# Performance work log

Measured on AMD Instinct MI355X. Metric: run time of the kernel, lower is better.

Reference implementation:

```python
import jax, jax.numpy as jnp
import numpy as np

B, S, H, NH = 2, 2048, 1024, 16
HD = H // NH
ROTARY_DIM = 64
EPS = 1e-5
MINUS_INF = -10000.0


def _apply_rotary(q, k, rotary_dim):
    # q, k: [B, S, NH, HD]; GPT-NeoX style rotate_half on first rotary_dim dims
    pos = jnp.arange(S, dtype=jnp.float32)
    inv_freq = 1.0 / (10000.0 ** (jnp.arange(0, rotary_dim, 2, dtype=jnp.float32) / rotary_dim))
    freqs = pos[:, None] * inv_freq[None, :]                      # [S, rd/2]
    cos = jnp.concatenate([jnp.cos(freqs)] * 2, -1)[None, :, None, :]  # [1,S,1,rd]
    sin = jnp.concatenate([jnp.sin(freqs)] * 2, -1)[None, :, None, :]

    def rot(t):
        t_rot, t_pass = t[..., :rotary_dim], t[..., rotary_dim:]
        t1, t2 = jnp.split(t_rot, 2, axis=-1)
        rotated = jnp.concatenate([-t2, t1], axis=-1)
        return jnp.concatenate([t_rot * cos + rotated * sin, t_pass], axis=-1)

    return rot(q), rot(k)


def setup_inputs() -> dict:
    key = jax.random.key(0)
    ks = jax.random.split(key, 6)
    w_scale = 0.02
    return {
        "x": jax.random.normal(ks[0], (B, S, H), jnp.float32),
        "input_mask": jnp.ones((B, S), jnp.int32),
        "norm_w": jnp.ones((H,), jnp.float32),
        "norm_b": jnp.zeros((H,), jnp.float32),
        "attn_qkvw": jax.random.normal(ks[1], (H, 3 * H), jnp.float32) * w_scale,
        "attn_qkvb": jax.random.normal(ks[2], (3 * H,), jnp.float32) * w_scale,
        "attn_ow": jax.random.normal(ks[3], (H, H), jnp.float32) * w_scale,
        "attn_ob": jax.random.normal(ks[4], (H,), jnp.float32) * w_scale,
    }


def reference(x, input_mask, norm_w, norm_b, attn_qkvw, attn_qkvb, attn_ow, attn_ob):
    # pre-layernorm (qkv_gemm path with config.pre_layer_norm)
    mu = x.mean(-1, keepdims=True)
    var = x.var(-1, keepdims=True)
    xn = (x - mu) * jax.lax.rsqrt(var + EPS) * norm_w + norm_b

    # fused QKV projection
    qkv = xn @ attn_qkvw + attn_qkvb                       # [B,S,3H]
    q, k, v = jnp.split(qkv, 3, axis=-1)
    q = q.reshape(B, S, NH, HD)
    k = k.reshape(B, S, NH, HD)
    v = v.reshape(B, S, NH, HD)

    # rotary embedding on q,k
    q, k = _apply_rotary(q, k, ROTARY_DIM)

    # scaled scores + mask bias (1 - mask) * -10000 + triangular masking
    scale = 1.0 / np.sqrt(HD).astype(np.float32)
    scores = jnp.einsum("bqhd,bkhd->bhqk", q, k) * scale   # [B,NH,S,S]
    mask_bias = (1.0 - input_mask.astype(scores.dtype)) * MINUS_INF
    scores = scores + mask_bias[:, None, None, :]
    causal = jnp.tril(jnp.ones((S, S), bool))
    scores = jnp.where(causal[None, None], scores, MINUS_INF)

    probs = jax.nn.softmax(scores, axis=-1)
    ctx = jnp.einsum("bhqk,bkhd->bqhd", probs, v).reshape(B, S, H)

    # output projection (vector_matmul + bias)
    return ctx @ attn_ow + attn_ob
```

## Files before the change

kernel.cpp:

```cpp
#include <hip/hip_runtime.h>
#include <hip/hip_bf16.h>

#define B_  2
#define S_  2048
#define H_  1024
#define NH_ 16
#define HD_ 64
#define T_  (B_*S_)
#define H3_ (3*H_)

typedef float  floatx4 __attribute__((ext_vector_type(4)));
typedef __bf16 bf16x8  __attribute__((ext_vector_type(8)));

__device__ inline unsigned short f2bf_rn(float f) {
    union { float f; unsigned int u; } v; v.f = f;
    unsigned int u = v.u;
    u += 0x7fffu + ((u >> 16) & 1u);
    return (unsigned short)(u >> 16);
}
__device__ inline floatx4 fzero4() { floatx4 v; v[0]=0.f; v[1]=0.f; v[2]=0.f; v[3]=0.f; return v; }

__device__ inline float bf2f(unsigned short u) {
    union { unsigned int i; float f; } x; x.i = ((unsigned int)u) << 16; return x.f;
}

__device__ inline unsigned int cvtpk_bf16(float lo, float hi) {
    unsigned int r;
    asm("v_cvt_pk_bf16_f32 %0, %1, %2" : "=v"(r) : "v"(lo), "v"(hi));
    return r;
}

__device__ inline void gload_lds16(const unsigned short* g, unsigned short* l) {
    __builtin_amdgcn_global_load_lds((const __attribute__((address_space(1))) unsigned int*)g,
                                     (__attribute__((address_space(3))) unsigned int*)l,
                                     16, 0, 0);
}

#define TLD 72
__global__ __launch_bounds__(256) void pre_k(const float* __restrict__ qkvw,
                                             const float* __restrict__ ow,
                                             unsigned short* __restrict__ qkvwT,
                                             unsigned short* __restrict__ owT,
                                             const float* __restrict__ x,
                                             const float* __restrict__ nw,
                                             const float* __restrict__ nb,
                                             unsigned short* __restrict__ xn) {
    const int tid = threadIdx.x;
    if (blockIdx.x < 1024) {
        __shared__ unsigned short Ts[64 * TLD];
        int id = blockIdx.x;
        const float* W; unsigned short* Wt; int N, nbs, kb;
        if (id < 768) { W = qkvw; Wt = qkvwT; N = H3_; nbs = (id % 48) * 64; kb = (id / 48) * 64; }
        else { id -= 768; W = ow; Wt = owT; N = H_; nbs = (id % 16) * 64; kb = (id / 16) * 64; }
        const int K = H_;
        #pragma unroll
        for (int p = 0; p < 4; p++) {
            const int krow = kb + p * 16 + (tid >> 4);
            const int ncol = (tid & 15) * 4;
            const float4 w = *reinterpret_cast<const float4*>(&W[(size_t)krow * N + nbs + ncol]);
            Ts[(ncol + 0) * TLD + p * 16 + (tid >> 4)] = f2bf_rn(w.x);
            Ts[(ncol + 1) * TLD + p * 16 + (tid >> 4)] = f2bf_rn(w.y);
            Ts[(ncol + 2) * TLD + p * 16 + (tid >> 4)] = f2bf_rn(w.z);
            Ts[(ncol + 3) * TLD + p * 16 + (tid >> 4)] = f2bf_rn(w.w);
        }
        __syncthreads();
        #pragma unroll
        for (int p = 0; p < 2; p++) {
            const int n = (tid >> 3) + p * 32;
            const int k8 = (tid & 7) * 8;
            const uint4 v = *reinterpret_cast<const uint4*>(&Ts[n * TLD + k8]);
            *reinterpret_cast<uint4*>(&Wt[(size_t)(nbs + n) * K + kb + k8]) = v;
        }
    } else {
        const int t = blockIdx.x - 1024;
        const float4 v = reinterpret_cast<const float4*>(x + (size_t)t * H_)[tid];
        float s  = v.x + v.y + v.z + v.w;
        float s2 = v.x*v.x + v.y*v.y + v.z*v.z + v.w*v.w;
        for (int off = 32; off > 0; off >>= 1) {
            s  += __shfl_down(s,  off, 64);
            s2 += __shfl_down(s2, off, 64);
        }
        __shared__ float red[8];
        const int wave = tid >> 6, lane = tid & 63;
        if (lane == 0) { red[wave] = s; red[4 + wave] = s2; }
        __syncthreads();
        if (tid == 0) {
            red[0] = red[0] + red[1] + red[2] + red[3];
            red[4] = red[4] + red[5] + red[6] + red[7];
        }
        __syncthreads();
        const float mean = red[0] * (1.f / H_);
        const float var  = red[4] * (1.f / H_) - mean * mean;
        const float rstd = rsqrtf(var + 1e-5f);
        const float4 wv = reinterpret_cast<const float4*>(nw)[tid];
        const float4 bv = reinterpret_cast<const float4*>(nb)[tid];
        ushort4 o = make_ushort4(f2bf_rn((v.x - mean) * rstd * wv.x + bv.x),
                                 f2bf_rn((v.y - mean) * rstd * wv.y + bv.y),
                                 f2bf_rn((v.z - mean) * rstd * wv.z + bv.z),
                                 f2bf_rn((v.w - mean) * rstd * wv.w + bv.w));
        reinterpret_cast<ushort4*>(xn + (size_t)t * H_)[tid] = o;
    }
}

__global__ __launch_bounds__(256) void gemm_qkv_k(const unsigned short* __restrict__ A,
                                                  const unsigned short* __restrict__ Bt,
                                                  const float* __restrict__ bias,
                                                  unsigned short* __restrict__ Qo,
                                                  unsigned short* __restrict__ Ko,
                                                  unsigned short* __restrict__ Vto) {
    __shared__ unsigned short As0[128 * 32], As1[128 * 32];
    __shared__ unsigned short Bs0[ 64 * 32], Bs1[ 64 * 32];

    const int tid  = threadIdx.x;
    const int lane = tid & 63;
    const int wave = tid >> 6;
    const int mBase = blockIdx.y * 128;
    const int nBase = blockIdx.x * 64;
    const int K = H_;

    const int srow = lane >> 2;
    const int scol = (lane & 3) * 8;
    const int mrow = lane & 15;
    const int koff = (lane >> 4) * 8;

    floatx4 acc[2][4];
    #pragma unroll
    for (int i = 0; i < 2; i++)
        #pragma unroll
        for (int j = 0; j < 4; j++) acc[i][j] = fzero4();

    for (int kb = 0; kb < K; kb += 64) {
        __syncthreads();
        #pragma unroll
        for (int p = 0; p < 2; p++) {
            const int r = wave * 16 + p * 64;
            const size_t ga = (size_t)(mBase + r + srow) * K + kb + scol;
            gload_lds16(&A[ga],      &As0[r * 32]);
            gload_lds16(&A[ga + 32], &As1[r * 32]);
        }
        {
            const int r = wave * 16;
            const size_t gb = (size_t)(nBase + r + srow) * K + kb + scol;
            gload_lds16(&Bt[gb],      &Bs0[r * 32]);
            gload_lds16(&Bt[gb + 32], &Bs1[r * 32]);
        }
        __syncthreads();

        #pragma unroll
        for (int half = 0; half < 2; half++) {
            const unsigned short* As = half ? As1 : As0;
            const unsigned short* Bs = half ? Bs1 : Bs0;
            bf16x8 afrag[2], bfrag[4];
            #pragma unroll
            for (int mt = 0; mt < 2; mt++)
                afrag[mt] = *reinterpret_cast<const bf16x8*>(&As[(wave * 32 + mt * 16 + mrow) * 32 + koff]);
            #pragma unroll
            for (int nt = 0; nt < 4; nt++)
                bfrag[nt] = *reinterpret_cast<const bf16x8*>(&Bs[(nt * 16 + mrow) * 32 + koff]);
            #pragma unroll
            for (int mt = 0; mt < 2; mt++)
                #pragma unroll
                for (int nt = 0; nt < 4; nt++)
                    acc[mt][nt] = __builtin_amdgcn_mfma_f32_16x16x32_bf16(afrag[mt], bfrag[nt], acc[mt][nt], 0, 0, 0);
        }
    }

    const int col0 = lane & 15;
    const int r0   = (lane >> 4) * 4;
    const int hg   = nBase >> 6;
    const int sec  = hg >> 4;
    const int h    = hg & 15;

    float bs[4];
    #pragma unroll
    for (int nt = 0; nt < 4; nt++) bs[nt] = bias[nBase + nt * 16 + col0];

    if (sec < 2) {
        unsigned short* dst = (sec == 0) ? Qo : Ko;
        const float if0 = __expf((float)col0        * (-0.2878231366f));
        const float if1 = __expf((float)(16 + col0) * (-0.2878231366f));
        #pragma unroll
        for (int mt = 0; mt < 2; mt++) {
            #pragma unroll
            for (int reg = 0; reg < 4; reg++) {
                const int t  = mBase + wave * 32 + mt * 16 + r0 + reg;
                const int bb = t >> 11;
                const int s  = t & (S_ - 1);
                float sn0, cs0, sn1, cs1;
                __sincosf((float)s * if0, &sn0, &cs0);
                __sincosf((float)s * if1, &sn1, &cs1);
                const float v0 = acc[mt][0][reg] + bs[0];
                const float v1 = acc[mt][1][reg] + bs[1];
                const float v2 = acc[mt][2][reg] + bs[2];
                const float v3 = acc[mt][3][reg] + bs[3];
                const float o0 = v0 * cs0 - v2 * sn0;
                const float o1 = v1 * cs1 - v3 * sn1;
                const float o2 = v2 * cs0 + v0 * sn0;
                const float o3 = v3 * cs1 + v1 * sn1;
                const size_t rb = ((size_t)(bb * NH_ + h) * S_ + s) * HD_;
                dst[rb +      col0] = f2bf_rn(o0);
                dst[rb + 16 + col0] = f2bf_rn(o1);
                dst[rb + 32 + col0] = f2bf_rn(o2);
                dst[rb + 48 + col0] = f2bf_rn(o3);
            }
        }
    } else {
        #pragma unroll
        for (int mt = 0; mt < 2; mt++) {
            const int t0 = mBase + wave * 32 + mt * 16 + r0;
            const int bb = t0 >> 11;
            const int s0 = t0 & (S_ - 1);
            #pragma unroll
            for (int nt = 0; nt < 4; nt++) {
                const int d = nt * 16 + col0;
                ushort4 o;
                o.x = f2bf_rn(acc[mt][nt][0] + bs[nt]);
                o.y = f2bf_rn(acc[mt][nt][1] + bs[nt]);
                o.z = f2bf_rn(acc[mt][nt][2] + bs[nt]);
                o.w = f2bf_rn(acc[mt][nt][3] + bs[nt]);
                *reinterpret_cast<ushort4*>(&Vto[((size_t)(bb * NH_ + h) * HD_ + d) * S_ + s0]) = o;
            }
        }
    }
}

__global__ __launch_bounds__(256) void gemm_proj_k(const unsigned short* __restrict__ A,
                                                   const unsigned short* __restrict__ Bt,
                                                   const float* __restrict__ bias,
                                                   float* __restrict__ Cf,
                                                   int M, int N, int K) {
    __shared__ unsigned short As0[128 * 32], As1[128 * 32];
    __shared__ unsigned short Bs0[ 64 * 32], Bs1[ 64 * 32];

    const int tid  = threadIdx.x;
    const int lane = tid & 63;
    const int wave = tid >> 6;
    const int id  = blockIdx.x;
    const int nid = (id & 7) * 64 + (id >> 3);
    const int mBase = (nid >> 4) * 128;
    const int nBase = (nid & 15) * 64;

    const int srow = lane >> 2;
    const int scol = (lane & 3) * 8;
    const int mrow = lane & 15;
    const int koff = (lane >> 4) * 8;

    floatx4 acc[2][4];
    #pragma unroll
    for (int i = 0; i < 2; i++)
        #pragma unroll
        for (int j = 0; j < 4; j++) acc[i][j] = fzero4();

    for (int kb = 0; kb < K; kb += 64) {
        __syncthreads();
        #pragma unroll
        for (int p = 0; p < 2; p++) {
            const int r = wave * 16 + p * 64;
            const size_t ga = (size_t)(mBase + r + srow) * K + kb + scol;
            gload_lds16(&A[ga],      &As0[r * 32]);
            gload_lds16(&A[ga + 32], &As1[r * 32]);
        }
        {
            const int r = wave * 16;
            const size_t gb = (size_t)(nBase + r + srow) * K + kb + scol;
            gload_lds16(&Bt[gb],      &Bs0[r * 32]);
            gload_lds16(&Bt[gb + 32], &Bs1[r * 32]);
        }
        __syncthreads();

        #pragma unroll
        for (int half = 0; half < 2; half++) {
            const unsigned short* As = half ? As1 : As0;
            const unsigned short* Bs = half ? Bs1 : Bs0;
            bf16x8 afrag[2], bfrag[4];
            #pragma unroll
            for (int mt = 0; mt < 2; mt++)
                afrag[mt] = *reinterpret_cast<const bf16x8*>(&As[(wave * 32 + mt * 16 + mrow) * 32 + koff]);
            #pragma unroll
            for (int nt = 0; nt < 4; nt++)
                bfrag[nt] = *reinterpret_cast<const bf16x8*>(&Bs[(nt * 16 + mrow) * 32 + koff]);
            #pragma unroll
            for (int mt = 0; mt < 2; mt++)
                #pragma unroll
                for (int nt = 0; nt < 4; nt++)
                    acc[mt][nt] = __builtin_amdgcn_mfma_f32_16x16x32_bf16(afrag[mt], bfrag[nt], acc[mt][nt], 0, 0, 0);
        }
    }

    const int col0 = lane & 15;
    const int r0   = (lane >> 4) * 4;
    #pragma unroll
    for (int mt = 0; mt < 2; mt++) {
        #pragma unroll
        for (int nt = 0; nt < 4; nt++) {
            const int gcol = nBase + nt * 16 + col0;
            const float bsv = bias[gcol];
            #pragma unroll
            for (int reg = 0; reg < 4; reg++) {
                const int grow = mBase + wave * 32 + mt * 16 + r0 + reg;
                Cf[(size_t)grow * N + gcol] = acc[mt][nt][reg] + bsv;
            }
        }
    }
}

#define ALD 72
#define SCL2 0.1803368801f
#define MNEG -14427.0f

__global__ __launch_bounds__(256, 4) void attn_k(const unsigned short* __restrict__ Q,
                                                 const unsigned short* __restrict__ Kg,
                                                 const unsigned short* __restrict__ Vt,
                                                 const int* __restrict__ mask,
                                                 unsigned short* __restrict__ ctx) {
    const int id = blockIdx.x;
    const int bh = id & 31;
    const int v  = 31 - (id >> 5);
    const int b  = bh >> 4;
    const int h  = bh & 15;
    const int tid  = threadIdx.x;
    const int lane = tid & 63;
    const int wave = tid >> 6;

    __shared__ unsigned short Ks [2][64 * ALD];
    __shared__ unsigned short Vts[2][64 * ALD];
    __shared__ unsigned short Mb [S_];

    const size_t base = (size_t)bh * S_ * HD_;
    const int qbase = v * 64 + wave * 16;
    const int r16  = lane & 15;
    const int koff = (lane >> 4) * 8;
    const int g8   = (lane >> 4) * 8;
    const int qcol = qbase + r16;

    {
        const int k0 = tid * 8;
        const int4 ma = *reinterpret_cast<const int4*>(&mask[b * S_ + k0]);
        const int4 mc = *reinterpret_cast<const int4*>(&mask[b * S_ + k0 + 4]);
        union { unsigned short us[8]; uint4 q; } pk;
        pk.us[0] = f2bf_rn((1.f - (float)ma.x) * MNEG);
        pk.us[1] = f2bf_rn((1.f - (float)ma.y) * MNEG);
        pk.us[2] = f2bf_rn((1.f - (float)ma.z) * MNEG);
        pk.us[3] = f2bf_rn((1.f - (float)ma.w) * MNEG);
        pk.us[4] = f2bf_rn((1.f - (float)mc.x) * MNEG);
        pk.us[5] = f2bf_rn((1.f - (float)mc.y) * MNEG);
        pk.us[6] = f2bf_rn((1.f - (float)mc.z) * MNEG);
        pk.us[7] = f2bf_rn((1.f - (float)mc.w) * MNEG);
        *reinterpret_cast<uint4*>(&Mb[k0]) = pk.q;
    }

    const bf16x8 qf0 = *reinterpret_cast<const bf16x8*>(&Q[base + (size_t)(qbase + r16) * HD_ + koff]);
    const bf16x8 qf1 = *reinterpret_cast<const bf16x8*>(&Q[base + (size_t)(qbase + r16) * HD_ + 32 + koff]);

    bf16x8 onesA;
    #pragma unroll
    for (int q = 0; q < 8; q++) onesA[q] = (__bf16)1.f;

    floatx4 Ot[4];
    #pragma unroll
    for (int db = 0; db < 4; db++) Ot[db] = fzero4();
    floatx4 Lacc = fzero4();

    const int srow = tid >> 3;
    const int scol = (tid & 7) * 8;
    const int pi = ((srow & 12) << 1) | (srow & 3) | (((srow >> 4) & 1) << 2);

    uint4 k00, k01, k10, k11, v00, v01, v10, v11;
#define PF_TILE(TT, KR0, KR1, VR0, VR1) do {                                                   \
        const int kb_ = (TT) * 64;                                                             \
        KR0 = *reinterpret_cast<const uint4*>(&Kg[base + (size_t)(kb_ + pi)      * HD_ + scol]); \
        KR1 = *reinterpret_cast<const uint4*>(&Kg[base + (size_t)(kb_ + 32 + pi) * HD_ + scol]); \
        VR0 = *reinterpret_cast<const uint4*>(&Vt[base + (size_t)srow        * S_ + kb_ + scol]);  \
        VR1 = *reinterpret_cast<const uint4*>(&Vt[base + (size_t)(srow + 32) * S_ + kb_ + scol]);  \
    } while (0)
#define PREFETCH_MACRO(MI) do {                                                                \
        const int t0_ = min(2 * (MI), v);                                                      \
        const int t1_ = min(2 * (MI) + 1, v);                                                  \
        PF_TILE(t0_, k00, k01, v00, v01);                                                      \
        PF_TILE(t1_, k10, k11, v10, v11);                                                      \
    } while (0)

    const int nmac = (v + 2) >> 1;
    PREFETCH_MACRO(0);

    for (int mi = 0; mi < nmac; mi++) {
        if (mi) __syncthreads();
        *reinterpret_cast<uint4*>(&Ks [0][ srow       * ALD + scol]) = k00;
        *reinterpret_cast<uint4*>(&Ks [0][(srow + 32) * ALD + scol]) = k01;
        *reinterpret_cast<uint4*>(&Ks [1][ srow       * ALD + scol]) = k10;
        *reinterpret_cast<uint4*>(&Ks [1][(srow + 32) * ALD + scol]) = k11;
        *reinterpret_cast<uint4*>(&Vts[0][ srow       * ALD + scol]) = v00;
        *reinterpret_cast<uint4*>(&Vts[0][(srow + 32) * ALD + scol]) = v01;
        *reinterpret_cast<uint4*>(&Vts[1][ srow       * ALD + scol]) = v10;
        *reinterpret_cast<uint4*>(&Vts[1][(srow + 32) * ALD + scol]) = v11;
        __syncthreads();
        if (mi + 1 < nmac) PREFETCH_MACRO(mi + 1);

        #pragma unroll
        for (int half = 0; half < 2; half++) {
            const int kt = 2 * mi + half;
            if (half && kt > v) continue;
            const int kb = kt * 64;
            const unsigned short* ks = Ks [half];
            const unsigned short* vs = Vts[half];

            const unsigned short* mbp = &Mb[kb + g8];
            const ushort4 b00 = *reinterpret_cast<const ushort4*>(mbp);
            const ushort4 b01 = *reinterpret_cast<const ushort4*>(mbp + 4);
            const ushort4 b10 = *reinterpret_cast<const ushort4*>(mbp + 32);
            const ushort4 b11 = *reinterpret_cast<const ushort4*>(mbp + 36);

            #pragma unroll
            for (int w = 0; w < 2; w++) {
                float p[2][4];
                #pragma unroll
                for (int ab = 0; ab < 2; ab++) {
                    const int nt = w * 2 + ab;
                    const bf16x8 kf0 = *reinterpret_cast<const bf16x8*>(&ks[(nt * 16 + r16) * ALD + koff]);
                    const bf16x8 kf1 = *reinterpret_cast<const bf16x8*>(&ks[(nt * 16 + r16) * ALD + 32 + koff]);
                    floatx4 c = fzero4();
                    c = __builtin_amdgcn_mfma_f32_16x16x32_bf16(kf0, qf0, c, 0, 0, 0);
                    c = __builtin_amdgcn_mfma_f32_16x16x32_bf16(kf1, qf1, c, 0, 0, 0);
                    const ushort4 bb = w ? (ab ? b11 : b10) : (ab ? b01 : b00);
                    const int kbase = kb + w * 32 + ab * 4 + g8;
                    float sc0 = c[0] * SCL2 + bf2f(bb.x);
                    float sc1 = c[1] * SCL2 + bf2f(bb.y);
                    float sc2 = c[2] * SCL2 + bf2f(bb.z);
                    float sc3 = c[3] * SCL2 + bf2f(bb.w);
                    if (kt == v) {
                        if (kbase + 0 > qcol) sc0 = MNEG;
                        if (kbase + 1 > qcol) sc1 = MNEG;
                        if (kbase + 2 > qcol) sc2 = MNEG;
                        if (kbase + 3 > qcol) sc3 = MNEG;
                    }
                    p[ab][0] = exp2f(sc0);
                    p[ab][1] = exp2f(sc1);
                    p[ab][2] = exp2f(sc2);
                    p[ab][3] = exp2f(sc3);
                }
                union { uint4 u; bf16x8 v; } pf;
                pf.u.x = cvtpk_bf16(p[0][0], p[0][1]);
                pf.u.y = cvtpk_bf16(p[0][2], p[0][3]);
                pf.u.z = cvtpk_bf16(p[1][0], p[1][1]);
                pf.u.w = cvtpk_bf16(p[1][2], p[1][3]);
                __builtin_amdgcn_s_setprio(1);
                #pragma unroll
                for (int db = 0; db < 4; db++) {
                    const bf16x8 vf = *reinterpret_cast<const bf16x8*>(&vs[(db * 16 + r16) * ALD + w * 32 + koff]);
                    Ot[db] = __builtin_amdgcn_mfma_f32_16x16x32_bf16(vf, pf.v, Ot[db], 0, 0, 0);
                }
                Lacc = __builtin_amdgcn_mfma_f32_16x16x32_bf16(onesA, pf.v, Lacc, 0, 0, 0);
                __builtin_amdgcn_s_setprio(0);
            }
        }
    }
#undef PREFETCH_MACRO
#undef PF_TILE

    const float rl = 1.f / Lacc[0];
    const int r4 = (lane >> 4) * 4;
    #pragma unroll
    for (int db = 0; db < 4; db++) {
        ushort4 o;
        o.x = f2bf_rn(Ot[db][0] * rl);
        o.y = f2bf_rn(Ot[db][1] * rl);
        o.z = f2bf_rn(Ot[db][2] * rl);
        o.w = f2bf_rn(Ot[db][3] * rl);
        *reinterpret_cast<ushort4*>(&ctx[((size_t)b * S_ + qcol) * H_ + h * HD_ + db * 16 + r4]) = o;
    }
}

extern "C" void kernel_launch(void* const* d_in, const int* in_sizes, int n_in,
                              void* d_out, int out_size, void* d_ws, size_t ws_size,
                              hipStream_t stream) {
    const float* x     = (const float*)d_in[0];
    const int*   mask  = (const int*)d_in[1];
    const float* normw = (const float*)d_in[2];
    const float* normb = (const float*)d_in[3];
    const float* qkvw  = (const float*)d_in[4];
    const float* qkvb  = (const float*)d_in[5];
    const float* ow    = (const float*)d_in[6];
    const float* ob    = (const float*)d_in[7];
    float* out = (float*)d_out;

    char* ws = (char*)d_ws;
    unsigned short* xn_bf   = (unsigned short*)(ws);
    unsigned short* qkvwT   = (unsigned short*)(ws + (8ull  << 20));
    unsigned short* owT     = (unsigned short*)(ws + (14ull << 20));
    unsigned short* Qb      = (unsigned short*)(ws + (16ull << 20));
    unsigned short* Kb      = (unsigned short*)(ws + (24ull << 20));
    unsigned short* Vtb     = (unsigned short*)(ws + (32ull << 20));
    unsigned short* ctx_bf  = (unsigned short*)(ws + (40ull << 20));

    pre_k<<<1024 + T_, 256, 0, stream>>>(qkvw, ow, qkvwT, owT, x, normw, normb, xn_bf);
    gemm_qkv_k<<<dim3(H3_ / 64, T_ / 128), 256, 0, stream>>>(xn_bf, qkvwT, qkvb, Qb, Kb, Vtb);
    attn_k<<<1024, 256, 0, stream>>>(Qb, Kb, Vtb, mask, ctx_bf);
    gemm_proj_k<<<512, 256, 0, stream>>>(ctx_bf, owT, ob, out, T_, H_, H_);
}
```

Baseline: 185.7 us.

## Fuse all stages into one persistent cooperative kernel with grid syncs

```diff
diff --git a/kernel.cpp b/kernel.cpp
--- a/kernel.cpp
+++ b/kernel.cpp
@@ -1,5 +1,8 @@
 #include <hip/hip_runtime.h>
 #include <hip/hip_bf16.h>
+#include <hip/hip_cooperative_groups.h>
+
+namespace cg = cooperative_groups;
 
 #define B_  2
 #define S_  2048
@@ -37,6 +40,458 @@
 }
 
 #define TLD 72
+#define ALD 72
+#define SCL2 0.1803368801f
+#define MNEG -14427.0f
+
+__device__ unsigned int g_tk[3];
+
+__global__ __launch_bounds__(256, 4) void fused_k(
+        const float* __restrict__ qkvw, const float* __restrict__ ow,
+        unsigned short* __restrict__ qkvwT, unsigned short* __restrict__ owT,
+        const float* __restrict__ x, const float* __restrict__ nw, const float* __restrict__ nb,
+        unsigned short* __restrict__ xn,
+        const float* __restrict__ qkvb,
+        unsigned short* __restrict__ Qg, unsigned short* __restrict__ Kgl, unsigned short* __restrict__ Vtg,
+        const int* __restrict__ mask, unsigned short* __restrict__ ctxb,
+        const float* __restrict__ ob, float* __restrict__ out)
+{
+    __shared__ __align__(16) char smem[37120];
+    __shared__ unsigned int s_tk;
+    const int bid = blockIdx.x;
+    const int G   = gridDim.x;
+    const int tid = threadIdx.x;
+    const int lane = tid & 63;
+    const int wave = tid >> 6;
+    cg::grid_group grid = cg::this_grid();
+
+    if (bid == 0 && tid < 3) g_tk[tid] = 0;
+
+    {
+        unsigned short* Ts = (unsigned short*)smem;
+        for (int c = bid; c < 1024; c += G) {
+            __syncthreads();
+            int id = c;
+            const float* W; unsigned short* Wt; int N, nbs, kb;
+            if (id < 768) { W = qkvw; Wt = qkvwT; N = H3_; nbs = (id % 48) * 64; kb = (id / 48) * 64; }
+            else { id -= 768; W = ow; Wt = owT; N = H_; nbs = (id % 16) * 64; kb = (id / 16) * 64; }
+            const int K = H_;
+            #pragma unroll
+            for (int p = 0; p < 4; p++) {
+                const int krow = kb + p * 16 + (tid >> 4);
+                const int ncol = (tid & 15) * 4;
+                const float4 w = *reinterpret_cast<const float4*>(&W[(size_t)krow * N + nbs + ncol]);
+                Ts[(ncol + 0) * TLD + p * 16 + (tid >> 4)] = f2bf_rn(w.x);
+                Ts[(ncol + 1) * TLD + p * 16 + (tid >> 4)] = f2bf_rn(w.y);
+                Ts[(ncol + 2) * TLD + p * 16 + (tid >> 4)] = f2bf_rn(w.z);
+                Ts[(ncol + 3) * TLD + p * 16 + (tid >> 4)] = f2bf_rn(w.w);
+            }
+            __syncthreads();
+            #pragma unroll
+            for (int p = 0; p < 2; p++) {
+                const int n = (tid >> 3) + p * 32;
+                const int k8 = (tid & 7) * 8;
+                const uint4 v = *reinterpret_cast<const uint4*>(&Ts[n * TLD + k8]);
+                *reinterpret_cast<uint4*>(&Wt[(size_t)(nbs + n) * K + kb + k8]) = v;
+            }
+        }
+    }
+
+    {
+        float* red = (float*)smem;
+        for (int t = bid; t < T_; t += G) {
+            __syncthreads();
+            const float4 v = reinterpret_cast<const float4*>(x + (size_t)t * H_)[tid];
+            float s  = v.x + v.y + v.z + v.w;
+            float s2 = v.x*v.x + v.y*v.y + v.z*v.z + v.w*v.w;
+            for (int off = 32; off > 0; off >>= 1) {
+                s  += __shfl_down(s,  off, 64);
+                s2 += __shfl_down(s2, off, 64);
+            }
+            if (lane == 0) { red[wave] = s; red[4 + wave] = s2; }
+            __syncthreads();
+            if (tid == 0) {
+                red[0] = red[0] + red[1] + red[2] + red[3];
+                red[4] = red[4] + red[5] + red[6] + red[7];
+            }
+            __syncthreads();
+            const float mean = red[0] * (1.f / H_);
+            const float var  = red[4] * (1.f / H_) - mean * mean;
+            const float rstd = rsqrtf(var + 1e-5f);
+            const float4 wv = reinterpret_cast<const float4*>(nw)[tid];
+            const float4 bv = reinterpret_cast<const float4*>(nb)[tid];
+            ushort4 o = make_ushort4(f2bf_rn((v.x - mean) * rstd * wv.x + bv.x),
+                                     f2bf_rn((v.y - mean) * rstd * wv.y + bv.y),
+                                     f2bf_rn((v.z - mean) * rstd * wv.z + bv.z),
+                                     f2bf_rn((v.w - mean) * rstd * wv.w + bv.w));
+            reinterpret_cast<ushort4*>(xn + (size_t)t * H_)[tid] = o;
+        }
+    }
+
+    __threadfence();
+    grid.sync();
+    __threadfence();
+
+    {
+        unsigned short* As0 = (unsigned short*)(smem);
+        unsigned short* As1 = (unsigned short*)(smem + 8192);
+        unsigned short* Bs0 = (unsigned short*)(smem + 16384);
+        unsigned short* Bs1 = (unsigned short*)(smem + 20480);
+        const int K = H_;
+        const int srow = lane >> 2;
+        const int scol = (lane & 3) * 8;
+        const int mrow = lane & 15;
+        const int koff = (lane >> 4) * 8;
+        const int col0 = lane & 15;
+        const int r0   = (lane >> 4) * 4;
+
+        for (;;) {
+            if (tid == 0) s_tk = atomicAdd(&g_tk[0], 1u);
+            __syncthreads();
+            const unsigned int t = s_tk;
+            if (t >= 1536u) break;
+            const int mBase = ((int)t / 48) * 128;
+            const int nBase = ((int)t % 48) * 64;
+
+            floatx4 acc[2][4];
+            #pragma unroll
+            for (int i = 0; i < 2; i++)
+                #pragma unroll
+                for (int j = 0; j < 4; j++) acc[i][j] = fzero4();
+
+            for (int kb = 0; kb < K; kb += 64) {
+                __syncthreads();
+                #pragma unroll
+                for (int p = 0; p < 2; p++) {
+                    const int r = wave * 16 + p * 64;
+                    const size_t ga = (size_t)(mBase + r + srow) * K + kb + scol;
+                    gload_lds16(&xn[ga],      &As0[r * 32]);
+                    gload_lds16(&xn[ga + 32], &As1[r * 32]);
+                }
+                {
+                    const int r = wave * 16;
+                    const size_t gb = (size_t)(nBase + r + srow) * K + kb + scol;
+                    gload_lds16(&qkvwT[gb],      &Bs0[r * 32]);
+                    gload_lds16(&qkvwT[gb + 32], &Bs1[r * 32]);
+                }
+                __syncthreads();
+
+                #pragma unroll
+                for (int half = 0; half < 2; half++) {
+                    const unsigned short* As = half ? As1 : As0;
+                    const unsigned short* Bs = half ? Bs1 : Bs0;
+                    bf16x8 afrag[2], bfrag[4];
+                    #pragma unroll
+                    for (int mt = 0; mt < 2; mt++)
+                        afrag[mt] = *reinterpret_cast<const bf16x8*>(&As[(wave * 32 + mt * 16 + mrow) * 32 + koff]);
+                    #pragma unroll
+                    for (int nt = 0; nt < 4; nt++)
+                        bfrag[nt] = *reinterpret_cast<const bf16x8*>(&Bs[(nt * 16 + mrow) * 32 + koff]);
+                    #pragma unroll
+                    for (int mt = 0; mt < 2; mt++)
+                        #pragma unroll
+                        for (int nt = 0; nt < 4; nt++)
+                            acc[mt][nt] = __builtin_amdgcn_mfma_f32_16x16x32_bf16(afrag[mt], bfrag[nt], acc[mt][nt], 0, 0, 0);
+                }
+            }
+
+            const int hg  = nBase >> 6;
+            const int sec = hg >> 4;
+            const int h   = hg & 15;
+
+            float bs[4];
+            #pragma unroll
+            for (int nt = 0; nt < 4; nt++) bs[nt] = qkvb[nBase + nt * 16 + col0];
+
+            if (sec < 2) {
+                unsigned short* dst = (sec == 0) ? Qg : Kgl;
+                const float if0 = __expf((float)col0        * (-0.2878231366f));
+                const float if1 = __expf((float)(16 + col0) * (-0.2878231366f));
+                #pragma unroll
+                for (int mt = 0; mt < 2; mt++) {
+                    #pragma unroll
+                    for (int reg = 0; reg < 4; reg++) {
+                        const int tt = mBase + wave * 32 + mt * 16 + r0 + reg;
+                        const int bb = tt >> 11;
+                        const int s  = tt & (S_ - 1);
+                        float sn0, cs0, sn1, cs1;
+                        __sincosf((float)s * if0, &sn0, &cs0);
+                        __sincosf((float)s * if1, &sn1, &cs1);
+                        const float v0 = acc[mt][0][reg] + bs[0];
+                        const float v1 = acc[mt][1][reg] + bs[1];
+                        const float v2 = acc[mt][2][reg] + bs[2];
+                        const float v3 = acc[mt][3][reg] + bs[3];
+                        const float o0 = v0 * cs0 - v2 * sn0;
+                        const float o1 = v1 * cs1 - v3 * sn1;
+                        const float o2 = v2 * cs0 + v0 * sn0;
+                        const float o3 = v3 * cs1 + v1 * sn1;
+                        const size_t rb = ((size_t)(bb * NH_ + h) * S_ + s) * HD_;
+                        dst[rb +      col0] = f2bf_rn(o0);
+                        dst[rb + 16 + col0] = f2bf_rn(o1);
+                        dst[rb + 32 + col0] = f2bf_rn(o2);
+                        dst[rb + 48 + col0] = f2bf_rn(o3);
+                    }
+                }
+            } else {
+                #pragma unroll
+                for (int mt = 0; mt < 2; mt++) {
+                    const int t0 = mBase + wave * 32 + mt * 16 + r0;
+                    const int bb = t0 >> 11;
+                    const int s0 = t0 & (S_ - 1);
+                    #pragma unroll
+                    for (int nt = 0; nt < 4; nt++) {
+                        const int d = nt * 16 + col0;
+                        ushort4 o;
+                        o.x = f2bf_rn(acc[mt][nt][0] + bs[nt]);
+                        o.y = f2bf_rn(acc[mt][nt][1] + bs[nt]);
+                        o.z = f2bf_rn(acc[mt][nt][2] + bs[nt]);
+                        o.w = f2bf_rn(acc[mt][nt][3] + bs[nt]);
+                        *reinterpret_cast<ushort4*>(&Vtg[((size_t)(bb * NH_ + h) * HD_ + d) * S_ + s0]) = o;
+                    }
+                }
+            }
+        }
+    }
+
+    __threadfence();
+    grid.sync();
+    __threadfence();
+
+    {
+        unsigned short* Ks0 = (unsigned short*)(smem);
+        unsigned short* Ks1 = (unsigned short*)(smem + 9216);
+        unsigned short* Vt0 = (unsigned short*)(smem + 18432);
+        unsigned short* Vt1 = (unsigned short*)(smem + 27648);
+        unsigned long long* Mb64 = (unsigned long long*)(smem + 36864);
+
+        const int r16  = lane & 15;
+        const int koff = (lane >> 4) * 8;
+        const int g8   = (lane >> 4) * 8;
+        const int srow = tid >> 3;
+        const int scol = (tid & 7) * 8;
+        const int pi = ((srow & 12) << 1) | (srow & 3) | (((srow >> 4) & 1) << 2);
+
+        for (;;) {
+            if (tid == 0) s_tk = atomicAdd(&g_tk[1], 1u);
+            __syncthreads();
+            const unsigned int u = s_tk;
+            if (u >= 1024u) break;
+            const int bh = (int)u & 31;
+            const int v  = 31 - ((int)u >> 5);
+            const int b  = bh >> 4;
+            const int h  = bh & 15;
+
+            const size_t base = (size_t)bh * S_ * HD_;
+            const int qbase = v * 64 + wave * 16;
+            const int qcol = qbase + r16;
+
+            #pragma unroll
+            for (int j = 0; j < 8; j++) {
+                const int widx = wave * 8 + j;
+                const int mv = mask[b * S_ + widx * 64 + lane];
+                const unsigned long long bal = __ballot(mv == 0);
+                if (lane == 0) Mb64[widx] = bal;
+            }
+
+            const bf16x8 qf0 = *reinterpret_cast<const bf16x8*>(&Qg[base + (size_t)(qbase + r16) * HD_ + koff]);
+            const bf16x8 qf1 = *reinterpret_cast<const bf16x8*>(&Qg[base + (size_t)(qbase + r16) * HD_ + 32 + koff]);
+
+            bf16x8 onesA;
+            #pragma unroll
+            for (int q = 0; q < 8; q++) onesA[q] = (__bf16)1.f;
+
+            floatx4 Ot[4];
+            #pragma unroll
+            for (int db = 0; db < 4; db++) Ot[db] = fzero4();
+            floatx4 Lacc = fzero4();
+
+            uint4 k00, k01, k10, k11, v00, v01, v10, v11;
+#define PF_TILE(TT, KR0, KR1, VR0, VR1) do {                                                     \
+        const int kb_ = (TT) * 64;                                                               \
+        KR0 = *reinterpret_cast<const uint4*>(&Kgl[base + (size_t)(kb_ + pi)      * HD_ + scol]); \
+        KR1 = *reinterpret_cast<const uint4*>(&Kgl[base + (size_t)(kb_ + 32 + pi) * HD_ + scol]); \
+        VR0 = *reinterpret_cast<const uint4*>(&Vtg[base + (size_t)srow        * S_ + kb_ + scol]); \
+        VR1 = *reinterpret_cast<const uint4*>(&Vtg[base + (size_t)(srow + 32) * S_ + kb_ + scol]); \
+    } while (0)
+#define PREFETCH_MACRO(MI) do {                                                                  \
+        const int t0_ = min(2 * (MI), v);                                                        \
+        const int t1_ = min(2 * (MI) + 1, v);                                                    \
+        PF_TILE(t0_, k00, k01, v00, v01);                                                        \
+        PF_TILE(t1_, k10, k11, v10, v11);                                                        \
+    } while (0)
+
+            const int nmac = (v + 2) >> 1;
+            PREFETCH_MACRO(0);
+
+            #pragma unroll 1
+            for (int mi = 0; mi < nmac; mi++) {
+                __syncthreads();
+                *reinterpret_cast<uint4*>(&Ks0[ srow       * ALD + scol]) = k00;
+                *reinterpret_cast<uint4*>(&Ks0[(srow + 32) * ALD + scol]) = k01;
+                *reinterpret_cast<uint4*>(&Ks1[ srow       * ALD + scol]) = k10;
+                *reinterpret_cast<uint4*>(&Ks1[(srow + 32) * ALD + scol]) = k11;
+                *reinterpret_cast<uint4*>(&Vt0[ srow       * ALD + scol]) = v00;
+                *reinterpret_cast<uint4*>(&Vt0[(srow + 32) * ALD + scol]) = v01;
+                *reinterpret_cast<uint4*>(&Vt1[ srow       * ALD + scol]) = v10;
+                *reinterpret_cast<uint4*>(&Vt1[(srow + 32) * ALD + scol]) = v11;
+                __syncthreads();
+                if (mi + 1 < nmac) PREFETCH_MACRO(mi + 1);
+
+                #pragma unroll
+                for (int half = 0; half < 2; half++) {
+                    const int kt = 2 * mi + half;
+                    if (half && kt > v) continue;
+                    const int kb = kt * 64;
+                    const unsigned short* ks = half ? Ks1 : Ks0;
+                    const unsigned short* vs = half ? Vt1 : Vt0;
+                    const unsigned long long mw = Mb64[kt];
+
+                    #pragma unroll
+                    for (int w = 0; w < 2; w++) {
+                        float p[2][4];
+                        #pragma unroll
+                        for (int ab = 0; ab < 2; ab++) {
+                            const int nt = w * 2 + ab;
+                            const bf16x8 kf0 = *reinterpret_cast<const bf16x8*>(&ks[(nt * 16 + r16) * ALD + koff]);
+                            const bf16x8 kf1 = *reinterpret_cast<const bf16x8*>(&ks[(nt * 16 + r16) * ALD + 32 + koff]);
+                            floatx4 c = fzero4();
+                            c = __builtin_amdgcn_mfma_f32_16x16x32_bf16(kf0, qf0, c, 0, 0, 0);
+                            c = __builtin_amdgcn_mfma_f32_16x16x32_bf16(kf1, qf1, c, 0, 0, 0);
+                            const int kbase = kb + w * 32 + ab * 4 + g8;
+                            const unsigned int mq = (unsigned int)(mw >> (w * 32 + ab * 4 + g8)) & 0xFu;
+                            float sc0 = c[0] * SCL2 + ((mq & 1u) ? MNEG : 0.f);
+                            float sc1 = c[1] * SCL2 + ((mq & 2u) ? MNEG : 0.f);
+                            float sc2 = c[2] * SCL2 + ((mq & 4u) ? MNEG : 0.f);
+                            float sc3 = c[3] * SCL2 + ((mq & 8u) ? MNEG : 0.f);
+                            if (kt == v) {
+                                if (kbase + 0 > qcol) sc0 = MNEG;
+                                if (kbase + 1 > qcol) sc1 = MNEG;
+                                if (kbase + 2 > qcol) sc2 = MNEG;
+                                if (kbase + 3 > qcol) sc3 = MNEG;
+                            }
+                            p[ab][0] = exp2f(sc0);
+                            p[ab][1] = exp2f(sc1);
+                            p[ab][2] = exp2f(sc2);
+                            p[ab][3] = exp2f(sc3);
+                        }
+                        union { uint4 u4; bf16x8 v8; } pf;
+                        pf.u4.x = cvtpk_bf16(p[0][0], p[0][1]);
+                        pf.u4.y = cvtpk_bf16(p[0][2], p[0][3]);
+                        pf.u4.z = cvtpk_bf16(p[1][0], p[1][1]);
+                        pf.u4.w = cvtpk_bf16(p[1][2], p[1][3]);
+                        __builtin_amdgcn_s_setprio(1);
+                        #pragma unroll
+                        for (int db = 0; db < 4; db++) {
+                            const bf16x8 vf = *reinterpret_cast<const bf16x8*>(&vs[(db * 16 + r16) * ALD + w * 32 + koff]);
+                            Ot[db] = __builtin_amdgcn_mfma_f32_16x16x32_bf16(vf, pf.v8, Ot[db], 0, 0, 0);
+                        }
+                        Lacc = __builtin_amdgcn_mfma_f32_16x16x32_bf16(onesA, pf.v8, Lacc, 0, 0, 0);
+                        __builtin_amdgcn_s_setprio(0);
+                    }
+                }
+            }
+#undef PREFETCH_MACRO
+#undef PF_TILE
+
+            const float rl = 1.f / Lacc[0];
+            const int r4 = (lane >> 4) * 4;
+            #pragma unroll
+            for (int db = 0; db < 4; db++) {
+                ushort4 o;
+                o.x = f2bf_rn(Ot[db][0] * rl);
+                o.y = f2bf_rn(Ot[db][1] * rl);
+                o.z = f2bf_rn(Ot[db][2] * rl);
+                o.w = f2bf_rn(Ot[db][3] * rl);
+                *reinterpret_cast<ushort4*>(&ctxb[((size_t)b * S_ + qcol) * H_ + h * HD_ + db * 16 + r4]) = o;
+            }
+        }
+    }
+
+    __threadfence();
+    grid.sync();
+    __threadfence();
+
+    {
+        unsigned short* As0 = (unsigned short*)(smem);
+        unsigned short* As1 = (unsigned short*)(smem + 8192);
+        unsigned short* Bs0 = (unsigned short*)(smem + 16384);
+        unsigned short* Bs1 = (unsigned short*)(smem + 20480);
+        const int K = H_, N = H_;
+        const int srow = lane >> 2;
+        const int scol = (lane & 3) * 8;
+        const int mrow = lane & 15;
+        const int koff = (lane >> 4) * 8;
+
+        for (;;) {
+            if (tid == 0) s_tk = atomicAdd(&g_tk[2], 1u);
+            __syncthreads();
+            const unsigned int t = s_tk;
+            if (t >= 512u) break;
+            const int nid = ((int)t & 7) * 64 + ((int)t >> 3);
+            const int mBase = (nid >> 4) * 128;
+            const int nBase = (nid & 15) * 64;
+
+            floatx4 acc[2][4];
+            #pragma unroll
+            for (int i = 0; i < 2; i++)
+                #pragma unroll
+                for (int j = 0; j < 4; j++) acc[i][j] = fzero4();
+
+            for (int kb = 0; kb < K; kb += 64) {
+                __syncthreads();
+                #pragma unroll
+                for (int p = 0; p < 2; p++) {
+                    const int r = wave * 16 + p * 64;
+                    const size_t ga = (size_t)(mBase + r + srow) * K + kb + scol;
+                    gload_lds16(&ctxb[ga],      &As0[r * 32]);
+                    gload_lds16(&ctxb[ga + 32], &As1[r * 32]);
+                }
+                {
+                    const int r = wave * 16;
+                    const size_t gb = (size_t)(nBase + r + srow) * K + kb + scol;
+                    gload_lds16(&owT[gb],      &Bs0[r * 32]);
+                    gload_lds16(&owT[gb + 32], &Bs1[r * 32]);
+                }
+                __syncthreads();
+
+                #pragma unroll
+                for (int half = 0; half < 2; half++) {
+                    const unsigned short* As = half ? As1 : As0;
+                    const unsigned short* Bs = half ? Bs1 : Bs0;
+                    bf16x8 afrag[2], bfrag[4];
+                    #pragma unroll
+                    for (int mt = 0; mt < 2; mt++)
+                        afrag[mt] = *reinterpret_cast<const bf16x8*>(&As[(wave * 32 + mt * 16 + mrow) * 32 + koff]);
+                    #pragma unroll
+                    for (int nt = 0; nt < 4; nt++)
+                        bfrag[nt] = *reinterpret_cast<const bf16x8*>(&Bs[(nt * 16 + mrow) * 32 + koff]);
+                    #pragma unroll
+                    for (int mt = 0; mt < 2; mt++)
+                        #pragma unroll
+                        for (int nt = 0; nt < 4; nt++)
+                            acc[mt][nt] = __builtin_amdgcn_mfma_f32_16x16x32_bf16(afrag[mt], bfrag[nt], acc[mt][nt], 0, 0, 0);
+                }
+            }
+
+            const int col0 = lane & 15;
+            const int r0   = (lane >> 4) * 4;
+            #pragma unroll
+            for (int mt = 0; mt < 2; mt++) {
+                #pragma unroll
+                for (int nt = 0; nt < 4; nt++) {
+                    const int gcol = nBase + nt * 16 + col0;
+                    const float bsv = ob[gcol];
+                    #pragma unroll
+                    for (int reg = 0; reg < 4; reg++) {
+                        const int grow = mBase + wave * 32 + mt * 16 + r0 + reg;
+                        out[(size_t)grow * N + gcol] = acc[mt][nt][reg] + bsv;
+                    }
+                }
+            }
+        }
+    }
+}
+
 __global__ __launch_bounds__(256) void pre_k(const float* __restrict__ qkvw,
                                              const float* __restrict__ ow,
                                              unsigned short* __restrict__ qkvwT,
@@ -303,10 +758,6 @@
         }
     }
 }
-
-#define ALD 72
-#define SCL2 0.1803368801f
-#define MNEG -14427.0f
 
 __global__ __launch_bounds__(256, 4) void attn_k(const unsigned short* __restrict__ Q,
                                                  const unsigned short* __restrict__ Kg,
@@ -492,6 +943,28 @@
     unsigned short* Vtb     = (unsigned short*)(ws + (32ull << 20));
     unsigned short* ctx_bf  = (unsigned short*)(ws + (40ull << 20));
 
+    static int coop_blocks = -1;
+    if (coop_blocks < 0) {
+        int nb = 0;
+        hipError_t e = hipOccupancyMaxActiveBlocksPerMultiprocessor(&nb, fused_k, 256, 0);
+        coop_blocks = (e == hipSuccess && nb >= 1) ? (nb > 4 ? 4 : nb) * 256 : 0;
+        if (coop_blocks > 1024) coop_blocks = 1024;
+    }
+    if (coop_blocks > 0) {
+        void* args[] = {
+            (void*)&qkvw, (void*)&ow, (void*)&qkvwT, (void*)&owT,
+            (void*)&x, (void*)&normw, (void*)&normb, (void*)&xn_bf,
+            (void*)&qkvb,
+            (void*)&Qb, (void*)&Kb, (void*)&Vtb,
+            (void*)&mask, (void*)&ctx_bf,
+            (void*)&ob, (void*)&out
+        };
+        if (hipLaunchCooperativeKernel((const void*)fused_k, dim3(coop_blocks), dim3(256),
+                                       args, 0, stream) == hipSuccess)
+            return;
+        coop_blocks = 0;
+    }
+
     pre_k<<<1024 + T_, 256, 0, stream>>>(qkvw, ow, qkvwT, owT, x, normw, normb, xn_bf);
     gemm_qkv_k<<<dim3(H3_ / 64, T_ / 128), 256, 0, stream>>>(xn_bf, qkvwT, qkvb, Qb, Kb, Vtb);
     attn_k<<<1024, 256, 0, stream>>>(Qb, Kb, Vtb, mask, ctx_bf);
```

Measured after the change: 642.2 us. +245.8%, slower.
